# Kernel optimization log

Hardware: AMD Instinct MI355X
Metric: run time of the kernel (lower is better)

Reference implementation:

```python
import jax, jax.numpy as jnp
import numpy as np

N, IN, HID, OUT, HD = 512, 256, 256, 256, 64  # n_agents, in_dim, hid_dim, out_dim, head_dim (out_dim // n_heads)


def _mlp2(x, w1, b1, w2, b2):
    return jax.nn.relu(x @ w1.T + b1) @ w2.T + b2


def setup_inputs():
    key = jax.random.key(0)
    ks = jax.random.split(key, 32)
    p = lambda i, shape: jax.random.normal(ks[i], shape, dtype=jnp.float32) * 0.05
    V = jax.random.normal(ks[0], (N, IN), dtype=jnp.float32)
    adj = jax.random.randint(ks[1], (N, N), 0, 2, dtype=jnp.int32)
    adj = adj.at[jnp.arange(N), jnp.arange(N)].set(1)  # self-loops so no softmax row is all -inf
    prev_hidden = jax.random.normal(ks[2], (N, HID), dtype=jnp.float32)
    return {
        "V": V, "adj": adj, "prev_hidden": prev_hidden,
        "W1": p(3, (HID, IN)), "sa0": p(4, (HID,)), "sa1": p(5, (HID,)),
        "ce_w1": p(6, (HID, 2 * IN)), "ce_b1": p(7, (HID,)), "ce_w2": p(8, (HD, HID)), "ce_b2": p(9, (HD,)),
        "ca0": p(10, (HD,)), "ca1": p(11, (HD,)),
        "te_w1": p(12, (HID, IN + HID)), "te_b1": p(13, (HID,)), "te_w2": p(14, (HD, HID)), "te_b2": p(15, (HD,)),
        "ta0": p(16, (HD,)), "ta1": p(17, (HD,)),
        "pe_w1": p(18, (HID, 3 * IN)), "pe_b1": p(19, (HID,)), "pe_w2": p(20, (HD, HID)), "pe_b2": p(21, (HD,)),
        "pa0": p(22, (HD,)), "pa1": p(23, (HD,)),
        "W2": p(24, (OUT, HID + 2 * HD + 1)), "op_w": p(25, (OUT, OUT)), "op_b": p(26, (OUT,)),
        "ln_g": jnp.ones((OUT,), jnp.float32), "ln_b": jnp.zeros((OUT,), jnp.float32),
    }


def _forward(V, adj, prev_hidden, W1, sa0, sa1, ce_w1, ce_b1, ce_w2, ce_b2, ca0, ca1,
             te_w1, te_b1, te_w2, te_b2, ta0, ta1, pe_w1, pe_b1, pe_w2, pe_b2, pa0, pa1,
             W2, op_w, op_b, ln_g, ln_b):
    neg = -jnp.inf
    # --- branch 1: standard GAT attention ---
    Wh1 = V @ W1.T                                             # (N, HID)
    s1 = (Wh1 @ sa0)[:, None] + (Wh1 @ sa1)[None, :]           # (N, N)
    s1 = jnp.where(adj == 0, neg, s1)
    H1 = jax.nn.softmax(s1, axis=1) @ Wh1                      # (N, HID)
    # --- branch 2: causal, all ordered pairs i != j ---
    wA, wB = ce_w1[:, :IN], ce_w1[:, IN:]
    h = jax.nn.relu((V @ wA.T)[:, None, :] + (V @ wB.T)[None, :, :] + ce_b1)  # (N, N, HID)
    f = h @ ce_w2.T + ce_b2                                    # (N, N, HD)
    s2 = jnp.where(jnp.eye(N, dtype=bool), neg, f @ (ca0 + ca1))
    a2 = jax.nn.softmax(s2.reshape(-1)).reshape(N, N)          # softmax over all off-diagonal pairs
    H2 = jnp.broadcast_to(jnp.einsum('ij,ijd->d', a2, f), (N, HD))
    # --- branch 3: temporal; (N,1) scores broadcast against (N,N) causal mask ---
    tf = _mlp2(jnp.concatenate([V, prev_hidden], -1), te_w1, te_b1, te_w2, te_b2)  # (N, HD)
    ts = tf @ (ta0 + ta1)                                      # (N,)
    cmask = jnp.triu(jnp.ones((N, N), dtype=bool), 1)
    s3 = jnp.where(cmask, neg, jnp.broadcast_to(ts[:, None], (N, N)))
    H3 = jax.nn.softmax(s3, axis=1) @ tf                       # (N, HD) == prefix means of tf
    # --- branch 4: cooperative; first two neighbors in index order (zeros if < 2) ---
    pos = jnp.where(adj == 1, jnp.arange(N)[None, :], N)
    srt = jnp.sort(pos, axis=1)
    i0, i1 = srt[:, 0], srt[:, 1]
    valid = (i1 < N)[:, None]
    n0 = jnp.where(valid, V[jnp.clip(i0, 0, N - 1)], 0.0)
    n1 = jnp.where(valid, V[jnp.clip(i1, 0, N - 1)], 0.0)
    cf = _mlp2(jnp.concatenate([V, n0, n1], -1), pe_w1, pe_b1, pe_w2, pe_b2)  # (N, HD)
    # torch: softmax over dim of size 1 -> all ones, alpha^T @ cf == column sums -> (HD,)
    # then unsqueezed to (HD,1) and zero-padded to (N,1) since HD < N  (faithful to source bug)
    H4v = cf.sum(axis=0)
    H4 = jnp.concatenate([H4v, jnp.zeros((N - HD,), V.dtype)])[:, None]       # (N, 1)
    # --- combine ---
    Hc = jnp.concatenate([H1, H2, H3, H4], axis=-1) @ W2.T     # (N, OUT)
    out = Hc @ op_w.T + op_b
    mu = out.mean(-1, keepdims=True)
    var = ((out - mu) ** 2).mean(-1, keepdims=True)
    y = (out - mu) / jnp.sqrt(var + 1e-5) * ln_g + ln_b        # LayerNorm, eps=1e-5
    return jax.nn.elu(y)                                       # dropout is identity in eval


def reference(V, adj, prev_hidden, W1, sa0, sa1, ce_w1, ce_b1, ce_w2, ce_b2, ca0, ca1,
              te_w1, te_b1, te_w2, te_b2, ta0, ta1, pe_w1, pe_b1, pe_w2, pe_b2, pa0, pa1,
              W2, op_w, op_b, ln_g, ln_b):
    return _forward(V, adj, prev_hidden, W1, sa0, sa1, ce_w1, ce_b1, ce_w2, ce_b2, ca0, ca1,
                    te_w1, te_b1, te_w2, te_b2, ta0, ta1, pe_w1, pe_b1, pe_w2, pe_b2, pa0, pa1,
                    W2, op_w, op_b, ln_g, ln_b)
```

## Files before the change

### kernel.cpp

```cpp
#include <hip/hip_runtime.h>

typedef unsigned short u16;

constexpr int kN   = 512;
constexpr int kIN  = 256;
constexpr int kHID = 256;
constexpr int kHD  = 64;
constexpr int kOUT = 256;

__device__ __forceinline__ float us2f(u16 u){
  union { unsigned int i; float f; } c; c.i = ((unsigned int)u) << 16; return c.f;
}
__device__ __forceinline__ u16 f2us(float f){
  union { float f; unsigned int i; } c; c.f = f;
  unsigned int r = c.i + 0x7fff + ((c.i >> 16) & 1);
  return (u16)(r >> 16);
}

__device__ bool probe_is_f32(const unsigned int* __restrict__ V){
  __shared__ int cnt;
  if (threadIdx.x == 0) cnt = 0;
  __syncthreads();
  int c = 0;
  for (int k = threadIdx.x; k < 4096; k += 256){
    float x = us2f((u16)(V[k] & 0xffffu));
    if (!(fabsf(x) <= 32.0f)) c++;
  }
  atomicAdd(&cnt, c);
  __syncthreads();
  return cnt > 64;
}

struct ConvArgs { const void* src[23]; float* dst[23]; int n[23]; };

__global__ __launch_bounds__(256) void k_conv(ConvArgs a, const unsigned int* __restrict__ Vraw,
                                              const int* __restrict__ adj, int* __restrict__ flag,
                                              float* __restrict__ Xp)
{
  int b = blockIdx.x, tid = threadIdx.x;
  bool f32 = probe_is_f32(Vraw);
  if (b < 256){
    if (b == 0 && tid == 0) *flag = f32 ? 1 : 0;
    int t = b*256 + tid;
    const int stride = 65536;
    for (int s = 0; s < 23; ++s){
      int n4 = a.n[s] >> 2;
      float4* d = (float4*)a.dst[s];
      if (f32){
        const float4* sf = (const float4*)a.src[s];
        for (int i = t; i < n4; i += stride) d[i] = sf[i];
      } else {
        const ushort4* sb = (const ushort4*)a.src[s];
        for (int i = t; i < n4; i += stride){
          ushort4 u = sb[i];
          d[i] = make_float4(us2f(u.x), us2f(u.y), us2f(u.z), us2f(u.w));
        }
      }
    }
  } else {
    __shared__ unsigned long long msk[8];
    __shared__ int sj[2];
    int i = b - 256;
    int w = tid >> 6, lane = tid & 63;
    unsigned long long m0 = __ballot(adj[(size_t)i*kN + tid] != 0);
    unsigned long long m1 = __ballot(adj[(size_t)i*kN + 256 + tid] != 0);
    if (lane == 0){ msk[w] = m0; msk[4 + w] = m1; }
    __syncthreads();
    if (tid == 0){
      int j0 = -1, j1 = -1;
      for (int c = 0; c < 8 && j1 < 0; ++c){
        unsigned long long m = msk[c];
        while (m && j1 < 0){
          int bb = __builtin_ctzll(m);
          int j = c*64 + bb;
          if (j0 < 0) j0 = j; else j1 = j;
          m &= m - 1;
        }
      }
      if (j1 < 0) j0 = -1;
      sj[0] = j0; sj[1] = j1;
    }
    __syncthreads();
    int j0 = sj[0], j1 = sj[1];
    const float* Vf = (const float*)Vraw;
    const u16*  Vb = (const u16*)Vraw;
    auto rdV = [&](int r, int k)->float{
      return f32 ? Vf[(size_t)r*kIN + k] : us2f(Vb[(size_t)r*kIN + k]);
    };
    Xp[(size_t)i*768 + tid]       = rdV(i, tid);
    Xp[(size_t)i*768 + 256 + tid] = (j0 >= 0) ? rdV(j0, tid) : 0.f;
    Xp[(size_t)i*768 + 512 + tid] = (j1 >= 0) ? rdV(j1, tid) : 0.f;
  }
}

__device__ __forceinline__ float blk_red(float v, float* tmp, bool isMax){
  int lane = threadIdx.x & 63, wv = threadIdx.x >> 6;
  #pragma unroll
  for (int o = 32; o > 0; o >>= 1){
    float t = __shfl_down(v, o, 64);
    v = isMax ? fmaxf(v, t) : (v + t);
  }
  __syncthreads();
  if (lane == 0) tmp[wv] = v;
  __syncthreads();
  float r = tmp[0];
  for (int i = 1; i < 4; ++i) r = isMax ? fmaxf(r, tmp[i]) : (r + tmp[i]);
  return r;
}

struct WSP {
  const int* adj; const int* flag; void* out;
  float *Vf,*prevf,*W1f,*sa1f,*cw1f,*cb1f,*cw2f,*cb2f,*ca0f,*ca1f;
  float *tw1f,*tb1f,*tw2f,*tb2f,*pw1f,*pb1f,*pw2f,*pb2f;
  float *W2f,*opwf,*opbf,*lngf,*lnbf;
  float *tw2t,*pw2t,*W2c,*W2midt,*w384v,*c2v;
  float *Wh1,*e1v,*minv,*invzv,*H1p,*Hc,*Am,*Bm,*uvec,*beta;
  float *s2,*maxp,*zp,*MZ,*gsum;
  float *htp0,*htp1,*hpp0,*hpp1,*hpp2,*hidden_t,*hidden_p;
  float *tfm,*cfm,*H4v,*Xp,*out2,*out3;
};

struct GSeg2 { const float* X; const float* W; float* C; int ldx, ldw, ldc, K; };
struct GArgs2 { GSeg2 s[8]; };

__global__ __launch_bounds__(256) void k_gemmA(GArgs2 ga)
{
  __shared__ __align__(16) float Xs[2][32][68];
  __shared__ __align__(16) float Ws[2][32][68];
  const GSeg2 sg = ga.s[blockIdx.y];
  const int tm = blockIdx.x & 7;
  const int tn = blockIdx.x >> 3;
  const int i0 = tm << 6;
  const int n0 = tn << 6;
  const int tid = threadIdx.x;

  const int xrow = tid >> 3;
  const int xk   = (tid & 7) << 2;
  const int rg = (tid >> 4) << 2;
  const int cg = (tid & 15) << 2;

  const float* Xb = sg.X + (size_t)i0 * sg.ldx;
  const float* Wb = sg.W + (size_t)n0 * sg.ldw;

  float4 xr0, xr1, wr0, wr1;
  auto loadT = [&](int kt){
    xr0 = *(const float4*)(Xb + (size_t)xrow * sg.ldx + kt + xk);
    xr1 = *(const float4*)(Xb + (size_t)(xrow+32) * sg.ldx + kt + xk);
    wr0 = *(const float4*)(Wb + (size_t)xrow * sg.ldw + kt + xk);
    wr1 = *(const float4*)(Wb + (size_t)(xrow+32) * sg.ldw + kt + xk);
  };
  auto writeT = [&](int bu){
    Xs[bu][xk+0][xrow] = xr0.x;  Xs[bu][xk+1][xrow] = xr0.y;
    Xs[bu][xk+2][xrow] = xr0.z;  Xs[bu][xk+3][xrow] = xr0.w;
    Xs[bu][xk+0][xrow+32] = xr1.x;  Xs[bu][xk+1][xrow+32] = xr1.y;
    Xs[bu][xk+2][xrow+32] = xr1.z;  Xs[bu][xk+3][xrow+32] = xr1.w;
    Ws[bu][xk+0][xrow]    = wr0.x; Ws[bu][xk+1][xrow]    = wr0.y;
    Ws[bu][xk+2][xrow]    = wr0.z; Ws[bu][xk+3][xrow]    = wr0.w;
    Ws[bu][xk+0][xrow+32] = wr1.x; Ws[bu][xk+1][xrow+32] = wr1.y;
    Ws[bu][xk+2][xrow+32] = wr1.z; Ws[bu][xk+3][xrow+32] = wr1.w;
  };

  loadT(0); writeT(0); __syncthreads();

  float acc[4][4] = {};
  const int nkt = sg.K >> 5;
  for (int t = 0; t < nkt; ++t){
    if (t + 1 < nkt) loadT((t + 1) << 5);
    const int bu = t & 1;
    #pragma unroll
    for (int kk = 0; kk < 32; ++kk){
      const float4 av = *(const float4*)&Xs[bu][kk][rg];
      const float4 bv = *(const float4*)&Ws[bu][kk][cg];
      acc[0][0]+=av.x*bv.x; acc[0][1]+=av.x*bv.y; acc[0][2]+=av.x*bv.z; acc[0][3]+=av.x*bv.w;
      acc[1][0]+=av.y*bv.x; acc[1][1]+=av.y*bv.y; acc[1][2]+=av.y*bv.z; acc[1][3]+=av.y*bv.w;
      acc[2][0]+=av.z*bv.x; acc[2][1]+=av.z*bv.y; acc[2][2]+=av.z*bv.z; acc[2][3]+=av.z*bv.w;
      acc[3][0]+=av.w*bv.x; acc[3][1]+=av.w*bv.y; acc[3][2]+=av.w*bv.z; acc[3][3]+=av.w*bv.w;
    }
    if (t + 1 < nkt) writeT((t + 1) & 1);
    __syncthreads();
  }

  #pragma unroll
  for (int ri = 0; ri < 4; ++ri)
    *(float4*)(sg.C + (size_t)(i0 + rg + ri) * sg.ldc + (n0 + cg)) =
      make_float4(acc[ri][0], acc[ri][1], acc[ri][2], acc[ri][3]);
}

struct GS32 { const float* X; const float* W; float* C; int ldx, ldw, ldc, K;
              const float* c2; const float* w384; const float* h4; };

__device__ __forceinline__ void gemm32_body(const GS32 sg, int tm, int tn, int tid,
                                            float* Xs, float* Ws)
{
  const int i0 = tm << 5, n0 = tn << 5;
  const int xrow = tid >> 3;
  const int xk = (tid & 7) << 2;
  const int rg = (tid >> 4) << 1;
  const int cg = (tid & 15) << 1;
  const float* Xb = sg.X + (size_t)i0 * sg.ldx;
  const float* Wb = sg.W + (size_t)n0 * sg.ldw;
  float h4r = 0.f;
  if (sg.h4){ int i = i0 + xrow; h4r = (i < 64) ? sg.h4[i] : 0.f; }
  float4 xr, wr;
  auto loadT = [&](int kt){
    xr = *(const float4*)(Xb + (size_t)xrow * sg.ldx + kt + xk);
    wr = *(const float4*)(Wb + (size_t)xrow * sg.ldw + kt + xk);
    if (sg.c2){
      float4 c = *(const float4*)(sg.c2 + kt + xk);
      float4 w3 = *(const float4*)(sg.w384 + kt + xk);
      xr.x += c.x + h4r*w3.x; xr.y += c.y + h4r*w3.y;
      xr.z += c.z + h4r*w3.z; xr.w += c.w + h4r*w3.w;
    }
  };
  auto writeT = [&](int bu){
    float* xs = Xs + bu*1152;
    xs[(xk+0)*36 + xrow] = xr.x; xs[(xk+1)*36 + xrow] = xr.y;
    xs[(xk+2)*36 + xrow] = xr.z; xs[(xk+3)*36 + xrow] = xr.w;
    float* wsp = Ws + bu*1152;
    wsp[(xk+0)*36 + xrow] = wr.x; wsp[(xk+1)*36 + xrow] = wr.y;
    wsp[(xk+2)*36 + xrow] = wr.z; wsp[(xk+3)*36 + xrow] = wr.w;
  };
  loadT(0); writeT(0); __syncthreads();
  float a00=0,a01=0,a10=0,a11=0;
  const int nkt = sg.K >> 5;
  for (int t = 0; t < nkt; ++t){
    if (t+1 < nkt) loadT((t+1) << 5);
    const float* xs = Xs + (t&1)*1152;
    const float* wsp = Ws + (t&1)*1152;
    #pragma unroll
    for (int kk = 0; kk < 32; ++kk){
      float2 av = *(const float2*)&xs[kk*36 + rg];
      float2 bv = *(const float2*)&wsp[kk*36 + cg];
      a00 += av.x*bv.x; a01 += av.x*bv.y;
      a10 += av.y*bv.x; a11 += av.y*bv.y;
    }
    if (t+1 < nkt) writeT((t+1)&1);
    __syncthreads();
  }
  float* cp = sg.C + (size_t)(i0+rg)*sg.ldc + n0 + cg;
  *(float2*)cp = make_float2(a00, a01);
  *(float2*)(cp + sg.ldc) = make_float2(a10, a11);
}

__global__ __launch_bounds__(256) void k_stage2(WSP w)
{
  __shared__ float st[64*65];
  int b = blockIdx.x, tid = threadIdx.x;
  if (b < 128){
    int f = b*256 + tid;
    int c4 = f & 63;
    {
      float4 a = ((const float4*)w.htp0)[f], bb = ((const float4*)w.htp1)[f];
      float4 bi = ((const float4*)w.tb1f)[c4];
      ((float4*)w.hidden_t)[f] = make_float4(
        fmaxf(a.x+bb.x+bi.x,0.f), fmaxf(a.y+bb.y+bi.y,0.f),
        fmaxf(a.z+bb.z+bi.z,0.f), fmaxf(a.w+bb.w+bi.w,0.f));
    }
    {
      float4 a = ((const float4*)w.hpp0)[f], bb = ((const float4*)w.hpp1)[f];
      float4 c = ((const float4*)w.hpp2)[f];
      float4 bi = ((const float4*)w.pb1f)[c4];
      ((float4*)w.hidden_p)[f] = make_float4(
        fmaxf(a.x+bb.x+c.x+bi.x,0.f), fmaxf(a.y+bb.y+c.y+bi.y,0.f),
        fmaxf(a.z+bb.z+c.z+bi.z,0.f), fmaxf(a.w+bb.w+c.w+bi.w,0.f));
    }
  } else if (b < 256){
    int r = (b-128)*4 + (tid >> 6), lane = tid & 63;
    float a = 0.f;
    for (int k = lane; k < kHID; k += 64) a += w.Wh1[(size_t)r*kHID + k] * w.sa1f[k];
    #pragma unroll
    for (int o = 32; o > 0; o >>= 1) a += __shfl_down(a, o, 64);
    if (lane == 0) w.e1v[r] = a;
  } else if (b == 256){
    if (tid < 64){ st[tid] = w.ca0f[tid] + w.ca1f[tid]; w.H4v[tid] = 0.f; }
    __syncthreads();
    float a = 0.f;
    for (int d = 0; d < kHD; ++d) a += w.cw2f[(size_t)d*kHID + tid] * st[d];
    w.uvec[tid] = a;
    if (tid == 0){
      float bsum = 0.f;
      for (int d = 0; d < kHD; ++d) bsum += w.cb2f[d] * st[d];
      *w.beta = bsum;
    }
  } else if (b < 259){
    const float* src = (b == 257) ? w.tw2f : w.pw2f;
    float* dst = (b == 257) ? w.tw2t : w.pw2t;
    for (int ch = 0; ch < 4; ++ch){
      __syncthreads();
      #pragma unroll
      for (int e = 0; e < 16; ++e){
        int lin = e*256 + tid;
        int r = lin >> 6, c = lin & 63;
        st[r*65 + c] = src[(size_t)r*256 + ch*64 + c];
      }
      __syncthreads();
      #pragma unroll
      for (int e = 0; e < 16; ++e){
        int lin = e*256 + tid;
        int kc = lin >> 6, dd = lin & 63;
        dst[(size_t)(ch*64 + kc)*64 + dd] = st[dd*65 + kc];
      }
    }
  } else if (b < 323){
    int o0 = (b - 259) * 4;
    for (int r = 0; r < 4; ++r){
      int o = o0 + r;
      const float* src = w.W2f + (size_t)o * 385;
      float* dst = w.W2c + (size_t)o * 320;
      for (int c = tid; c < 320; c += 256)
        dst[c] = src[(c < 256) ? c : c + 64];
    }
  } else if (b < 339){
    int d0 = (b - 323) * 4;
    #pragma unroll
    for (int dd = 0; dd < 4; ++dd)
      w.W2midt[(size_t)(d0+dd)*256 + tid] = w.W2f[(size_t)tid*385 + 256 + d0 + dd];
  } else {
    w.w384v[tid] = w.W2f[(size_t)tid*385 + 384];
  }
}

__global__ __launch_bounds__(256) void k_stage3(WSP w)
{
  __shared__ __align__(16) float smem3[4*256 + 256];
  int b = blockIdx.x, tid = threadIdx.x;
  if (b < 64){
    int m = b >> 5, grp = b & 31;
    const float* X  = m ? w.hidden_p : w.hidden_t;
    const float* Wt = m ? w.pw2t : w.tw2t;
    const float* bi = m ? w.pb2f : w.tb2f;
    float* C = m ? w.cfm : w.tfm;
    int i0 = grp*16 + (tid >> 6)*4;
    int d = tid & 63;
    const float* x0 = X + (size_t)i0*256;
    const float* x1 = x0 + 256;
    const float* x2 = x0 + 512;
    const float* x3 = x0 + 768;
    float a0=0.f, a1=0.f, a2=0.f, a3=0.f;
    for (int k = 0; k < 256; k += 4){
      float w0 = Wt[(size_t)(k+0)*64 + d];
      float w1 = Wt[(size_t)(k+1)*64 + d];
      float w2 = Wt[(size_t)(k+2)*64 + d];
      float w3 = Wt[(size_t)(k+3)*64 + d];
      float4 f0 = *(const float4*)(x0 + k);
      float4 f1 = *(const float4*)(x1 + k);
      float4 f2 = *(const float4*)(x2 + k);
      float4 f3 = *(const float4*)(x3 + k);
      a0 += f0.x*w0 + f0.y*w1 + f0.z*w2 + f0.w*w3;
      a1 += f1.x*w0 + f1.y*w1 + f1.z*w2 + f1.w*w3;
      a2 += f2.x*w0 + f2.y*w1 + f2.z*w2 + f2.w*w3;
      a3 += f3.x*w0 + f3.y*w1 + f3.z*w2 + f3.w*w3;
    }
    float bd = bi[d];
    C[(size_t)(i0+0)*64 + d] = a0 + bd;
    C[(size_t)(i0+1)*64 + d] = a1 + bd;
    C[(size_t)(i0+2)*64 + d] = a2 + bd;
    C[(size_t)(i0+3)*64 + d] = a3 + bd;
  } else if (b < 576){
    float* red = smem3;
    int i = b - 64;
    int m0 = w.adj[(size_t)i*kN + tid];
    int m1 = w.adj[(size_t)i*kN + tid + 256];
    float ea = w.e1v[tid], eb = w.e1v[tid+256];
    float v0 = m0 ? ea : -1e30f;
    float v1 = m1 ? eb : -1e30f;
    float m = blk_red(fmaxf(v0, v1), red, true);
    float z = blk_red((m0 ? expf(ea-m) : 0.f) + (m1 ? expf(eb-m) : 0.f), red, false);
    if (tid == 0){ w.minv[i] = m; w.invzv[i] = 1.0f / z; }
  } else {
    float* aib = smem3;
    float* uu  = smem3 + 1024;
    int q = b - 576;
    int i0 = (q & 127) * 4, j0 = (q >> 7) * 64;
    int wv = tid >> 6, lane = tid & 63;
    uu[tid] = w.uvec[tid];
    float b1v = w.cb1f[tid];
    #pragma unroll
    for (int r = 0; r < 4; ++r) aib[r*256 + tid] = w.Am[(size_t)(i0+r)*kHID + tid] + b1v;
    __syncthreads();
    int i = i0 + wv, j = j0 + lane;
    const float4* bp = (const float4*)(w.Bm + (size_t)j*kHID);
    float acc = *w.beta;
    #pragma unroll 8
    for (int k4 = 0; k4 < kHID/4; ++k4){
      float4 bv = bp[k4];
      float4 a4 = *(const float4*)&aib[wv*256 + k4*4];
      float4 u4 = *(const float4*)&uu[k4*4];
      acc += fmaxf(a4.x+bv.x,0.f)*u4.x + fmaxf(a4.y+bv.y,0.f)*u4.y
           + fmaxf(a4.z+bv.z,0.f)*u4.z + fmaxf(a4.w+bv.w,0.f)*u4.w;
    }
    if (j == i) acc = -1e30f;
    w.s2[(size_t)i*kN + j] = acc;
    float m = acc;
    #pragma unroll
    for (int o = 32; o > 0; o >>= 1) m = fmaxf(m, __shfl_down(m, o, 64));
    m = __shfl(m, 0, 64);
    float e = expf(acc - m);
    #pragma unroll
    for (int o = 32; o > 0; o >>= 1) e += __shfl_down(e, o, 64);
    if (lane == 0){
      int pb = q*4 + wv;
      w.maxp[pb] = m; w.zp[pb] = e;
    }
  }
}

__global__ __launch_bounds__(256) void k_stage4(WSP w)
{
  __shared__ __align__(16) float smem[272];
  int b = blockIdx.x, tid = threadIdx.x;
  if (b < 8){
    int d = tid & 63, sub = tid >> 6;
    int r0 = b*64 + sub*16;
    float s = 0.f;
    #pragma unroll
    for (int e = 0; e < 16; ++e) s += w.cfm[(size_t)(r0+e)*kHD + d];
    smem[sub*64 + d] = s;
    __syncthreads();
    if (tid < 64)
      atomicAdd(&w.H4v[tid], smem[tid] + smem[64+tid] + smem[128+tid] + smem[192+tid]);
  } else if (b < 1032){
    float* wt = smem;
    int q = b - 8;
    int i0 = (q & 127) * 4, jt = q >> 7, j0 = jt * 64;
    {
      int r = tid >> 6, jj = tid & 63;
      int j = j0 + jj;
      wt[r*64 + jj] = w.adj[(size_t)(i0+r)*kN + j]
                    ? expf(w.e1v[j] - w.minv[i0+r]) * w.invzv[i0+r] : 0.f;
    }
    __syncthreads();
    float a0=0,a1=0,a2=0,a3=0;
    #pragma unroll 4
    for (int jj = 0; jj < 64; ++jj){
      float wh = w.Wh1[(size_t)(j0+jj)*kHID + tid];
      a0 += wt[jj]*wh; a1 += wt[64+jj]*wh; a2 += wt[128+jj]*wh; a3 += wt[192+jj]*wh;
    }
    size_t base = ((size_t)jt*kN + i0)*kHID + tid;
    w.H1p[base]          = a0;
    w.H1p[base + kHID]   = a1;
    w.H1p[base + 2*kHID] = a2;
    w.H1p[base + 3*kHID] = a3;
  } else {
    float* red = smem;
    float m = -1e30f;
    #pragma unroll
    for (int r = 0; r < 16; ++r) m = fmaxf(m, w.maxp[tid + 256*r]);
    m = blk_red(m, red, true);
    float z = 0.f;
    #pragma unroll
    for (int r = 0; r < 16; ++r) z += w.zp[tid + 256*r] * expf(w.maxp[tid + 256*r] - m);
    z = blk_red(z, red, false);
    if (tid == 0){ w.MZ[0] = m; w.MZ[1] = z; }
    w.gsum[tid] = 0.f;
  }
}

__global__ __launch_bounds__(256) void k_stage5(WSP w)
{
  __shared__ __align__(16) char smem[1536];
  int b = blockIdx.x, tid = threadIdx.x;
  if (b < 1024){
    float* wt = (float*)smem;
    int i0 = (b & 31) * 16, j0 = (b >> 5) * 16;
    float M = w.MZ[0], invZ = 1.0f / w.MZ[1];
    {
      int r = tid >> 4, c = tid & 15;
      wt[r*16 + c] = expf(w.s2[(size_t)(i0+r)*kN + (j0+c)] - M) * invZ;
    }
    float b1v = w.cb1f[tid];
    float aib[16];
    #pragma unroll
    for (int r = 0; r < 16; ++r) aib[r] = w.Am[(size_t)(i0+r)*kHID + tid] + b1v;
    __syncthreads();
    float acc = 0.f;
    for (int j = 0; j < 16; ++j){
      float bj = w.Bm[(size_t)(j0+j)*kHID + tid];
      #pragma unroll
      for (int r = 0; r < 16; ++r)
        acc += wt[r*16 + j] * fmaxf(aib[r] + bj, 0.f);
    }
    atomicAdd(&w.gsum[tid], acc);
  } else if (b < 1536){
    int i = b - 1024;
    float s = 0.f;
    #pragma unroll
    for (int jt = 0; jt < 8; ++jt)
      s += w.H1p[((size_t)jt*kN + i)*kHID + tid];
    w.Hc[(size_t)i*320 + tid] = s;
  } else {
    int d = b - 1536;
    int lane = tid & 63, wv = tid >> 6;
    float v0 = w.tfm[(size_t)(2*tid)*kHD + d];
    float v1 = w.tfm[(size_t)(2*tid+1)*kHD + d];
    float s = v0 + v1;
    float x = s;
    #pragma unroll
    for (int off = 1; off < 64; off <<= 1){
      float y = __shfl_up(x, off, 64);
      if (lane >= off) x += y;
    }
    float* wsum = (float*)smem;
    if (lane == 63) wsum[wv] = x;
    __syncthreads();
    float base = 0.f;
    for (int k = 0; k < wv; ++k) base += wsum[k];
    float excl = base + x - s;
    w.Hc[(size_t)(2*tid)*320 + 256 + d]   = (excl + v0) / (float)(2*tid + 1);
    w.Hc[(size_t)(2*tid+1)*320 + 256 + d] = (excl + s)  / (float)(2*tid + 2);
  }
}

__global__ __launch_bounds__(256) void k_out2g(WSP w)
{
  __shared__ __align__(16) char smem[18432];
  int b = blockIdx.x, tid = threadIdx.x;
  if (b < 128){
    GS32 sg{w.Hc, w.W2c, w.out2, 320, 320, 256, 320, nullptr, nullptr, nullptr};
    gemm32_body(sg, b & 15, b >> 4, tid, (float*)smem, (float*)(smem + 9216));
  } else {
    float* gs  = (float*)smem;
    float* part= (float*)(smem + 1024);
    float* h2s = (float*)(smem + 2048);
    gs[tid] = w.gsum[tid];
    __syncthreads();
    int dd = tid >> 2, q = tid & 3;
    float a = 0.f;
    for (int kk = 0; kk < 64; ++kk){
      int k = q*64 + kk;
      a += gs[k] * w.cw2f[(size_t)dd*kHID + k];
    }
    part[dd*4 + q] = a;
    __syncthreads();
    if (tid < kHD)
      h2s[tid] = w.cb2f[tid] + part[tid*4] + part[tid*4+1] + part[tid*4+2] + part[tid*4+3];
    __syncthreads();
    float c = 0.f;
    for (int d = 0; d < kHD; ++d) c += h2s[d] * w.W2midt[(size_t)d*256 + tid];
    w.c2v[tid] = c;
  }
}

__global__ __launch_bounds__(256) void k_out3g(WSP w)
{
  __shared__ __align__(16) char smem[18432];
  GS32 sg{w.out2, w.opwf, w.out3, 256, 256, 256, 256, w.c2v, w.w384v, w.H4v};
  gemm32_body(sg, blockIdx.x & 15, blockIdx.x >> 4, threadIdx.x, (float*)smem, (float*)(smem + 9216));
}

__global__ __launch_bounds__(256) void k_final(WSP w)
{
  int b = blockIdx.x, tid = threadIdx.x;
  int row = b*4 + (tid >> 6), lane = tid & 63;
  float4 v = *(const float4*)(w.out3 + (size_t)row*kOUT + lane*4);
  float4 pb = *(const float4*)(w.opbf + lane*4);
  v.x += pb.x; v.y += pb.y; v.z += pb.z; v.w += pb.w;
  float s = v.x + v.y + v.z + v.w;
  #pragma unroll
  for (int o = 32; o > 0; o >>= 1) s += __shfl_xor(s, o, 64);
  float mu = s * (1.0f/kOUT);
  float dx = v.x-mu, dy = v.y-mu, dz = v.z-mu, dw = v.w-mu;
  float ss = dx*dx + dy*dy + dz*dz + dw*dw;
  #pragma unroll
  for (int o = 32; o > 0; o >>= 1) ss += __shfl_xor(ss, o, 64);
  float rs = rsqrtf(ss * (1.0f/kOUT) + 1e-5f);
  float4 g = *(const float4*)(w.lngf + lane*4);
  float4 be = *(const float4*)(w.lnbf + lane*4);
  float y0 = dx*rs*g.x + be.x, y1 = dy*rs*g.y + be.y;
  float y2 = dz*rs*g.z + be.z, y3 = dw*rs*g.w + be.w;
  y0 = (y0 > 0.f) ? y0 : expm1f(y0);
  y1 = (y1 > 0.f) ? y1 : expm1f(y1);
  y2 = (y2 > 0.f) ? y2 : expm1f(y2);
  y3 = (y3 > 0.f) ? y3 : expm1f(y3);
  if (*w.flag){
    *(float4*)((float*)w.out + (size_t)row*kOUT + lane*4) = make_float4(y0,y1,y2,y3);
  } else {
    ushort4 u; u.x = f2us(y0); u.y = f2us(y1); u.z = f2us(y2); u.w = f2us(y3);
    ((ushort4*)w.out)[(size_t)row*64 + lane] = u;
  }
}

extern "C" void kernel_launch(void* const* d_in, const int* in_sizes, int n_in,
                              void* d_out, int out_size, void* d_ws, size_t ws_size,
                              hipStream_t stream)
{
  const void* V     = d_in[0];
  const int*  adj   = (const int*)d_in[1];
  const void* prev  = d_in[2];
  const void* W1    = d_in[3];
  const void* sa1   = d_in[5];
  const void* ce_w1 = d_in[6];
  const void* ce_b1 = d_in[7];
  const void* ce_w2 = d_in[8];
  const void* ce_b2 = d_in[9];
  const void* ca0   = d_in[10];
  const void* ca1   = d_in[11];
  const void* te_w1 = d_in[12];
  const void* te_b1 = d_in[13];
  const void* te_w2 = d_in[14];
  const void* te_b2 = d_in[15];
  const void* pe_w1 = d_in[18];
  const void* pe_b1 = d_in[19];
  const void* pe_w2 = d_in[20];
  const void* pe_b2 = d_in[21];
  const void* W2    = d_in[24];
  const void* op_w  = d_in[25];
  const void* op_b  = d_in[26];
  const void* ln_g  = d_in[27];
  const void* ln_b  = d_in[28];

  float* ws  = (float*)d_ws;
  int*  flag = (int*)ws;
  float* p   = ws + 16;
  float* Vf   = p; p += 131072;
  float* prevf= p; p += 131072;
  float* W1f  = p; p += 65536;
  float* sa1f = p; p += 256;
  float* cw1f = p; p += 131072;
  float* cb1f = p; p += 256;
  float* cw2f = p; p += 16384;
  float* cb2f = p; p += 64;
  float* ca0f = p; p += 64;
  float* ca1f = p; p += 64;
  float* tw1f = p; p += 131072;
  float* tb1f = p; p += 256;
  float* tw2f = p; p += 16384;
  float* tb2f = p; p += 64;
  float* pw1f = p; p += 196608;
  float* pb1f = p; p += 256;
  float* pw2f = p; p += 16384;
  float* pb2f = p; p += 64;
  float* W2f  = p; p += 98560;
  float* opwf = p; p += 65536;
  float* opbf = p; p += 256;
  float* lngf = p; p += 256;
  float* lnbf = p; p += 256;
  float* tw2t = p; p += 16384;
  float* pw2t = p; p += 16384;
  float* W2c  = p; p += 81920;
  float* W2midt = p; p += 16384;
  float* w384v  = p; p += 256;
  float* c2v    = p; p += 256;
  float* Wh1      = p; p += 131072;
  float* e1v      = p; p += 512;
  float* minv     = p; p += 512;
  float* invzv    = p; p += 512;
  float* H1p      = p; p += 1048576;
  float* Hc       = p; p += 163840;
  float* Am       = p; p += 131072;
  float* Bm       = p; p += 131072;
  float* uvec     = p; p += 256;
  float* beta     = p; p += 16;
  float* s2       = p; p += 262144;
  float* maxp     = p; p += 4096;
  float* zpart    = p; p += 4096;
  float* MZ       = p; p += 16;
  float* gsum     = p; p += 256;
  float* htp0     = p; p += 131072;
  float* htp1     = p; p += 131072;
  float* hpp0     = p; p += 131072;
  float* hpp1     = p; p += 131072;
  float* hpp2     = p; p += 131072;
  float* hidden_t = p; p += 131072;
  float* hidden_p = p; p += 131072;
  float* tfm      = p; p += 32768;
  float* cfm      = p; p += 32768;
  float* H4v      = p; p += 64;
  float* Xp       = p; p += 393216;
  float* out2     = p; p += 131072;
  float* out3     = p; p += 131072;

  WSP w;
  w.adj = adj; w.flag = flag; w.out = d_out;
  w.Vf=Vf; w.prevf=prevf; w.W1f=W1f; w.sa1f=sa1f; w.cw1f=cw1f; w.cb1f=cb1f;
  w.cw2f=cw2f; w.cb2f=cb2f; w.ca0f=ca0f; w.ca1f=ca1f;
  w.tw1f=tw1f; w.tb1f=tb1f; w.tw2f=tw2f; w.tb2f=tb2f;
  w.pw1f=pw1f; w.pb1f=pb1f; w.pw2f=pw2f; w.pb2f=pb2f;
  w.W2f=W2f; w.opwf=opwf; w.opbf=opbf; w.lngf=lngf; w.lnbf=lnbf;
  w.tw2t=tw2t; w.pw2t=pw2t; w.W2c=W2c; w.W2midt=W2midt; w.w384v=w384v; w.c2v=c2v;
  w.Wh1=Wh1; w.e1v=e1v; w.minv=minv; w.invzv=invzv; w.H1p=H1p; w.Hc=Hc;
  w.Am=Am; w.Bm=Bm; w.uvec=uvec; w.beta=beta;
  w.s2=s2; w.maxp=maxp; w.zp=zpart; w.MZ=MZ; w.gsum=gsum;
  w.htp0=htp0; w.htp1=htp1; w.hpp0=hpp0; w.hpp1=hpp1; w.hpp2=hpp2;
  w.hidden_t=hidden_t; w.hidden_p=hidden_p;
  w.tfm=tfm; w.cfm=cfm; w.H4v=H4v; w.Xp=Xp; w.out2=out2; w.out3=out3;

  {
    ConvArgs ca;
    const void* srcs[23] = {V, prev, W1, sa1, ce_w1, ce_b1, ce_w2, ce_b2, ca0, ca1,
                            te_w1, te_b1, te_w2, te_b2, pe_w1, pe_b1, pe_w2, pe_b2,
                            W2, op_w, op_b, ln_g, ln_b};
    float* dsts[23] = {Vf, prevf, W1f, sa1f, cw1f, cb1f, cw2f, cb2f, ca0f, ca1f,
                       tw1f, tb1f, tw2f, tb2f, pw1f, pb1f, pw2f, pb2f,
                       W2f, opwf, opbf, lngf, lnbf};
    int ns[23] = {131072, 131072, 65536, 256, 131072, 256, 16384, 64, 64, 64,
                  131072, 256, 16384, 64, 196608, 256, 16384, 64,
                  98560, 65536, 256, 256, 256};
    for (int s = 0; s < 23; ++s){ ca.src[s] = srcs[s]; ca.dst[s] = dsts[s]; ca.n[s] = ns[s]; }
    k_conv<<<768, 256, 0, stream>>>(ca, (const unsigned int*)V, adj, flag, Xp);
  }

  {
    GArgs2 g{};
    g.s[0] = {Vf,       W1f,        Wh1,  256, 256, 256, 256};
    g.s[1] = {Vf,       cw1f,       Am,   256, 512, 256, 256};
    g.s[2] = {Vf,       cw1f + 256, Bm,   256, 512, 256, 256};
    g.s[3] = {Vf,       tw1f,       htp0, 256, 512, 256, 256};
    g.s[4] = {prevf,    tw1f + 256, htp1, 256, 512, 256, 256};
    g.s[5] = {Xp,       pw1f,       hpp0, 768, 768, 256, 256};
    g.s[6] = {Xp + 256, pw1f + 256, hpp1, 768, 768, 256, 256};
    g.s[7] = {Xp + 512, pw1f + 512, hpp2, 768, 768, 256, 256};
    k_gemmA<<<dim3(32, 8), 256, 0, stream>>>(g);
  }

  k_stage2<<<340, 256, 0, stream>>>(w);

  k_stage3<<<1600, 256, 0, stream>>>(w);

  k_stage4<<<1033, 256, 0, stream>>>(w);

  k_stage5<<<1600, 256, 0, stream>>>(w);

  k_out2g<<<129, 256, 0, stream>>>(w);

  k_out3g<<<128, 256, 0, stream>>>(w);

  k_final<<<128, 256, 0, stream>>>(w);
}
```

Measured before the change: 244.7 us.

## Compute GAT branch as softmax-weight matrix times Wh1 GEMM, fuse e1 into gemmA

The e1 = Wh1·sa1 dot products are now accumulated with atomics in the epilogue of the Wh1 GEMM, and the per-row softmax max and sum move into stage2. Stage3 writes a dense normalized attention matrix. H1 is then computed by a tiled GEMM (with a new K-major weight load path) straight into Hc, replacing the 8-way partial products and the separate reduction pass. This removes the large H1p scratch buffer and its reduction. In exchange it adds a 512x512 weight matrix write, float atomics that make e1 summation order nondeterministic, and a launch reordering that puts the out2 GEMM in stage5 with a separate single-block k_h2c.

```diff
diff --git a/kernel.cpp b/kernel.cpp
--- a/kernel.cpp
+++ b/kernel.cpp
@@ -35,12 +35,15 @@
 
 __global__ __launch_bounds__(256) void k_conv(ConvArgs a, const unsigned int* __restrict__ Vraw,
                                               const int* __restrict__ adj, int* __restrict__ flag,
-                                              float* __restrict__ Xp)
+                                              float* __restrict__ Xp, float* __restrict__ e1v)
 {
   int b = blockIdx.x, tid = threadIdx.x;
   bool f32 = probe_is_f32(Vraw);
   if (b < 256){
-    if (b == 0 && tid == 0) *flag = f32 ? 1 : 0;
+    if (b == 0){
+      if (tid == 0) *flag = f32 ? 1 : 0;
+      e1v[tid] = 0.f; e1v[tid + 256] = 0.f;
+    }
     int t = b*256 + tid;
     const int stride = 65536;
     for (int s = 0; s < 23; ++s){
@@ -114,14 +117,14 @@
   float *tw1f,*tb1f,*tw2f,*tb2f,*pw1f,*pb1f,*pw2f,*pb2f;
   float *W2f,*opwf,*opbf,*lngf,*lnbf;
   float *tw2t,*pw2t,*W2c,*W2midt,*w384v,*c2v;
-  float *Wh1,*e1v,*minv,*invzv,*H1p,*Hc,*Am,*Bm,*uvec,*beta;
+  float *Wh1,*e1v,*minv,*invzv,*wadj,*Hc,*Am,*Bm,*uvec,*beta;
   float *s2,*maxp,*zp,*MZ,*gsum;
   float *htp0,*htp1,*hpp0,*hpp1,*hpp2,*hidden_t,*hidden_p;
   float *tfm,*cfm,*H4v,*Xp,*out2,*out3;
 };
 
 struct GSeg2 { const float* X; const float* W; float* C; int ldx, ldw, ldc, K; };
-struct GArgs2 { GSeg2 s[8]; };
+struct GArgs2 { GSeg2 s[8]; const float* sa1; float* e1; };
 
 __global__ __launch_bounds__(256) void k_gemmA(GArgs2 ga)
 {
@@ -184,10 +187,24 @@
   for (int ri = 0; ri < 4; ++ri)
     *(float4*)(sg.C + (size_t)(i0 + rg + ri) * sg.ldc + (n0 + cg)) =
       make_float4(acc[ri][0], acc[ri][1], acc[ri][2], acc[ri][3]);
+
+  if (blockIdx.y == 0){
+    int cb = n0 + cg;
+    float s0 = ga.sa1[cb], s1 = ga.sa1[cb+1], s2v = ga.sa1[cb+2], s3 = ga.sa1[cb+3];
+    #pragma unroll
+    for (int ri = 0; ri < 4; ++ri){
+      float v = acc[ri][0]*s0 + acc[ri][1]*s1 + acc[ri][2]*s2v + acc[ri][3]*s3;
+      v += __shfl_xor(v, 1, 16);
+      v += __shfl_xor(v, 2, 16);
+      v += __shfl_xor(v, 4, 16);
+      v += __shfl_xor(v, 8, 16);
+      if ((tid & 15) == 0) atomicAdd(&ga.e1[i0 + rg + ri], v);
+    }
+  }
 }
 
 struct GS32 { const float* X; const float* W; float* C; int ldx, ldw, ldc, K;
-              const float* c2; const float* w384; const float* h4; };
+              const float* c2; const float* w384; const float* h4; int bkn; };
 
 __device__ __forceinline__ void gemm32_body(const GS32 sg, int tm, int tn, int tid,
                                             float* Xs, float* Ws)
@@ -198,13 +215,14 @@
   const int rg = (tid >> 4) << 1;
   const int cg = (tid & 15) << 1;
   const float* Xb = sg.X + (size_t)i0 * sg.ldx;
-  const float* Wb = sg.W + (size_t)n0 * sg.ldw;
+  const float* Wb = sg.bkn ? (sg.W + n0) : (sg.W + (size_t)n0 * sg.ldw);
   float h4r = 0.f;
   if (sg.h4){ int i = i0 + xrow; h4r = (i < 64) ? sg.h4[i] : 0.f; }
   float4 xr, wr;
   auto loadT = [&](int kt){
     xr = *(const float4*)(Xb + (size_t)xrow * sg.ldx + kt + xk);
-    wr = *(const float4*)(Wb + (size_t)xrow * sg.ldw + kt + xk);
+    if (sg.bkn) wr = *(const float4*)(Wb + (size_t)(kt + xrow) * sg.ldw + xk);
+    else        wr = *(const float4*)(Wb + (size_t)xrow * sg.ldw + kt + xk);
     if (sg.c2){
       float4 c = *(const float4*)(sg.c2 + kt + xk);
       float4 w3 = *(const float4*)(sg.w384 + kt + xk);
@@ -217,8 +235,13 @@
     xs[(xk+0)*36 + xrow] = xr.x; xs[(xk+1)*36 + xrow] = xr.y;
     xs[(xk+2)*36 + xrow] = xr.z; xs[(xk+3)*36 + xrow] = xr.w;
     float* wsp = Ws + bu*1152;
-    wsp[(xk+0)*36 + xrow] = wr.x; wsp[(xk+1)*36 + xrow] = wr.y;
-    wsp[(xk+2)*36 + xrow] = wr.z; wsp[(xk+3)*36 + xrow] = wr.w;
+    if (sg.bkn){
+      wsp[xrow*36 + xk+0] = wr.x; wsp[xrow*36 + xk+1] = wr.y;
+      wsp[xrow*36 + xk+2] = wr.z; wsp[xrow*36 + xk+3] = wr.w;
+    } else {
+      wsp[(xk+0)*36 + xrow] = wr.x; wsp[(xk+1)*36 + xrow] = wr.y;
+      wsp[(xk+2)*36 + xrow] = wr.z; wsp[(xk+3)*36 + xrow] = wr.w;
+    }
   };
   loadT(0); writeT(0); __syncthreads();
   float a00=0,a01=0,a10=0,a11=0;
@@ -264,14 +287,18 @@
         fmaxf(a.x+bb.x+c.x+bi.x,0.f), fmaxf(a.y+bb.y+c.y+bi.y,0.f),
         fmaxf(a.z+bb.z+c.z+bi.z,0.f), fmaxf(a.w+bb.w+c.w+bi.w,0.f));
     }
-  } else if (b < 256){
-    int r = (b-128)*4 + (tid >> 6), lane = tid & 63;
-    float a = 0.f;
-    for (int k = lane; k < kHID; k += 64) a += w.Wh1[(size_t)r*kHID + k] * w.sa1f[k];
-    #pragma unroll
-    for (int o = 32; o > 0; o >>= 1) a += __shfl_down(a, o, 64);
-    if (lane == 0) w.e1v[r] = a;
-  } else if (b == 256){
+  } else if (b < 640){
+    float* red = st;
+    int i = b - 128;
+    int m0 = w.adj[(size_t)i*kN + tid];
+    int m1 = w.adj[(size_t)i*kN + tid + 256];
+    float ea = w.e1v[tid], eb = w.e1v[tid+256];
+    float v0 = m0 ? ea : -1e30f;
+    float v1 = m1 ? eb : -1e30f;
+    float m = blk_red(fmaxf(v0, v1), red, true);
+    float z = blk_red((m0 ? expf(ea-m) : 0.f) + (m1 ? expf(eb-m) : 0.f), red, false);
+    if (tid == 0){ w.minv[i] = m; w.invzv[i] = 1.0f / z; }
+  } else if (b == 640){
     if (tid < 64){ st[tid] = w.ca0f[tid] + w.ca1f[tid]; w.H4v[tid] = 0.f; }
     __syncthreads();
     float a = 0.f;
@@ -282,9 +309,9 @@
       for (int d = 0; d < kHD; ++d) bsum += w.cb2f[d] * st[d];
       *w.beta = bsum;
     }
-  } else if (b < 259){
-    const float* src = (b == 257) ? w.tw2f : w.pw2f;
-    float* dst = (b == 257) ? w.tw2t : w.pw2t;
+  } else if (b < 643){
+    const float* src = (b == 641) ? w.tw2f : w.pw2f;
+    float* dst = (b == 641) ? w.tw2t : w.pw2t;
     for (int ch = 0; ch < 4; ++ch){
       __syncthreads();
       #pragma unroll
@@ -301,8 +328,8 @@
         dst[(size_t)(ch*64 + kc)*64 + dd] = st[dd*65 + kc];
       }
     }
-  } else if (b < 323){
-    int o0 = (b - 259) * 4;
+  } else if (b < 707){
+    int o0 = (b - 643) * 4;
     for (int r = 0; r < 4; ++r){
       int o = o0 + r;
       const float* src = w.W2f + (size_t)o * 385;
@@ -310,8 +337,8 @@
       for (int c = tid; c < 320; c += 256)
         dst[c] = src[(c < 256) ? c : c + 64];
     }
-  } else if (b < 339){
-    int d0 = (b - 323) * 4;
+  } else if (b < 723){
+    int d0 = (b - 707) * 4;
     #pragma unroll
     for (int dd = 0; dd < 4; ++dd)
       w.W2midt[(size_t)(d0+dd)*256 + tid] = w.W2f[(size_t)tid*385 + 256 + d0 + dd];
@@ -357,16 +384,12 @@
     C[(size_t)(i0+2)*64 + d] = a2 + bd;
     C[(size_t)(i0+3)*64 + d] = a3 + bd;
   } else if (b < 576){
-    float* red = smem3;
     int i = b - 64;
-    int m0 = w.adj[(size_t)i*kN + tid];
-    int m1 = w.adj[(size_t)i*kN + tid + 256];
-    float ea = w.e1v[tid], eb = w.e1v[tid+256];
-    float v0 = m0 ? ea : -1e30f;
-    float v1 = m1 ? eb : -1e30f;
-    float m = blk_red(fmaxf(v0, v1), red, true);
-    float z = blk_red((m0 ? expf(ea-m) : 0.f) + (m1 ? expf(eb-m) : 0.f), red, false);
-    if (tid == 0){ w.minv[i] = m; w.invzv[i] = 1.0f / z; }
+    float mi = w.minv[i], zi = w.invzv[i];
+    w.wadj[(size_t)i*kN + tid] =
+      w.adj[(size_t)i*kN + tid] ? expf(w.e1v[tid] - mi) * zi : 0.f;
+    w.wadj[(size_t)i*kN + tid + 256] =
+      w.adj[(size_t)i*kN + tid + 256] ? expf(w.e1v[tid+256] - mi) * zi : 0.f;
   } else {
     float* aib = smem3;
     float* uu  = smem3 + 1024;
@@ -407,42 +430,44 @@
 
 __global__ __launch_bounds__(256) void k_stage4(WSP w)
 {
-  __shared__ __align__(16) float smem[272];
+  __shared__ __align__(16) char smem[18432];
   int b = blockIdx.x, tid = threadIdx.x;
-  if (b < 8){
+  if (b < 128){
+    GS32 sg{w.wadj, w.Wh1, w.Hc, 512, 256, 320, 512, nullptr, nullptr, nullptr, 1};
+    gemm32_body(sg, b & 15, b >> 4, tid, (float*)smem, (float*)(smem + 9216));
+  } else if (b < 192){
+    int d = b - 128;
+    int lane = tid & 63, wv = tid >> 6;
+    float v0 = w.tfm[(size_t)(2*tid)*kHD + d];
+    float v1 = w.tfm[(size_t)(2*tid+1)*kHD + d];
+    float s = v0 + v1;
+    float x = s;
+    #pragma unroll
+    for (int off = 1; off < 64; off <<= 1){
+      float y = __shfl_up(x, off, 64);
+      if (lane >= off) x += y;
+    }
+    float* wsum = (float*)smem;
+    if (lane == 63) wsum[wv] = x;
+    __syncthreads();
+    float base = 0.f;
+    for (int k = 0; k < wv; ++k) base += wsum[k];
+    float excl = base + x - s;
+    w.Hc[(size_t)(2*tid)*320 + 256 + d]   = (excl + v0) / (float)(2*tid + 1);
+    w.Hc[(size_t)(2*tid+1)*320 + 256 + d] = (excl + s)  / (float)(2*tid + 2);
+  } else if (b < 200){
+    float* sm = (float*)smem;
     int d = tid & 63, sub = tid >> 6;
-    int r0 = b*64 + sub*16;
+    int r0 = (b-192)*64 + sub*16;
     float s = 0.f;
     #pragma unroll
     for (int e = 0; e < 16; ++e) s += w.cfm[(size_t)(r0+e)*kHD + d];
-    smem[sub*64 + d] = s;
+    sm[sub*64 + d] = s;
     __syncthreads();
     if (tid < 64)
-      atomicAdd(&w.H4v[tid], smem[tid] + smem[64+tid] + smem[128+tid] + smem[192+tid]);
-  } else if (b < 1032){
-    float* wt = smem;
-    int q = b - 8;
-    int i0 = (q & 127) * 4, jt = q >> 7, j0 = jt * 64;
-    {
-      int r = tid >> 6, jj = tid & 63;
-      int j = j0 + jj;
-      wt[r*64 + jj] = w.adj[(size_t)(i0+r)*kN + j]
-                    ? expf(w.e1v[j] - w.minv[i0+r]) * w.invzv[i0+r] : 0.f;
-    }
-    __syncthreads();
-    float a0=0,a1=0,a2=0,a3=0;
-    #pragma unroll 4
-    for (int jj = 0; jj < 64; ++jj){
-      float wh = w.Wh1[(size_t)(j0+jj)*kHID + tid];
-      a0 += wt[jj]*wh; a1 += wt[64+jj]*wh; a2 += wt[128+jj]*wh; a3 += wt[192+jj]*wh;
-    }
-    size_t base = ((size_t)jt*kN + i0)*kHID + tid;
-    w.H1p[base]          = a0;
-    w.H1p[base + kHID]   = a1;
-    w.H1p[base + 2*kHID] = a2;
-    w.H1p[base + 3*kHID] = a3;
+      atomicAdd(&w.H4v[tid], sm[tid] + sm[64+tid] + sm[128+tid] + sm[192+tid]);
   } else {
-    float* red = smem;
+    float* red = (float*)smem;
     float m = -1e30f;
     #pragma unroll
     for (int r = 0; r < 16; ++r) m = fmaxf(m, w.maxp[tid + 256*r]);
@@ -458,7 +483,7 @@
 
 __global__ __launch_bounds__(256) void k_stage5(WSP w)
 {
-  __shared__ __align__(16) char smem[1536];
+  __shared__ __align__(16) char smem[18432];
   int b = blockIdx.x, tid = threadIdx.x;
   if (b < 1024){
     float* wt = (float*)smem;
@@ -481,70 +506,41 @@
         acc += wt[r*16 + j] * fmaxf(aib[r] + bj, 0.f);
     }
     atomicAdd(&w.gsum[tid], acc);
-  } else if (b < 1536){
-    int i = b - 1024;
-    float s = 0.f;
-    #pragma unroll
-    for (int jt = 0; jt < 8; ++jt)
-      s += w.H1p[((size_t)jt*kN + i)*kHID + tid];
-    w.Hc[(size_t)i*320 + tid] = s;
   } else {
-    int d = b - 1536;
-    int lane = tid & 63, wv = tid >> 6;
-    float v0 = w.tfm[(size_t)(2*tid)*kHD + d];
-    float v1 = w.tfm[(size_t)(2*tid+1)*kHD + d];
-    float s = v0 + v1;
-    float x = s;
-    #pragma unroll
-    for (int off = 1; off < 64; off <<= 1){
-      float y = __shfl_up(x, off, 64);
-      if (lane >= off) x += y;
-    }
-    float* wsum = (float*)smem;
-    if (lane == 63) wsum[wv] = x;
-    __syncthreads();
-    float base = 0.f;
-    for (int k = 0; k < wv; ++k) base += wsum[k];
-    float excl = base + x - s;
-    w.Hc[(size_t)(2*tid)*320 + 256 + d]   = (excl + v0) / (float)(2*tid + 1);
-    w.Hc[(size_t)(2*tid+1)*320 + 256 + d] = (excl + s)  / (float)(2*tid + 2);
-  }
-}
-
-__global__ __launch_bounds__(256) void k_out2g(WSP w)
+    int q = b - 1024;
+    GS32 sg{w.Hc, w.W2c, w.out2, 320, 320, 256, 320, nullptr, nullptr, nullptr, 0};
+    gemm32_body(sg, q & 15, q >> 4, tid, (float*)smem, (float*)(smem + 9216));
+  }
+}
+
+__global__ void k_h2c(WSP w)
+{
+  __shared__ float gs[kHID];
+  __shared__ float part[kHD][4];
+  __shared__ float h2s[kHD];
+  int tid = threadIdx.x;
+  gs[tid] = w.gsum[tid];
+  __syncthreads();
+  int dd = tid >> 2, q = tid & 3;
+  float a = 0.f;
+  for (int kk = 0; kk < 64; ++kk){
+    int k = q*64 + kk;
+    a += gs[k] * w.cw2f[(size_t)dd*kHID + k];
+  }
+  part[dd][q] = a;
+  __syncthreads();
+  if (tid < kHD)
+    h2s[tid] = w.cb2f[tid] + part[tid][0] + part[tid][1] + part[tid][2] + part[tid][3];
+  __syncthreads();
+  float c = 0.f;
+  for (int d = 0; d < kHD; ++d) c += h2s[d] * w.W2midt[(size_t)d*256 + tid];
+  w.c2v[tid] = c;
+}
+
+__global__ __launch_bounds__(256) void k_out3g(WSP w)
 {
   __shared__ __align__(16) char smem[18432];
-  int b = blockIdx.x, tid = threadIdx.x;
-  if (b < 128){
-    GS32 sg{w.Hc, w.W2c, w.out2, 320, 320, 256, 320, nullptr, nullptr, nullptr};
-    gemm32_body(sg, b & 15, b >> 4, tid, (float*)smem, (float*)(smem + 9216));
-  } else {
-    float* gs  = (float*)smem;
-    float* part= (float*)(smem + 1024);
-    float* h2s = (float*)(smem + 2048);
-    gs[tid] = w.gsum[tid];
-    __syncthreads();
-    int dd = tid >> 2, q = tid & 3;
-    float a = 0.f;
-    for (int kk = 0; kk < 64; ++kk){
-      int k = q*64 + kk;
-      a += gs[k] * w.cw2f[(size_t)dd*kHID + k];
-    }
-    part[dd*4 + q] = a;
-    __syncthreads();
-    if (tid < kHD)
-      h2s[tid] = w.cb2f[tid] + part[tid*4] + part[tid*4+1] + part[tid*4+2] + part[tid*4+3];
-    __syncthreads();
-    float c = 0.f;
-    for (int d = 0; d < kHD; ++d) c += h2s[d] * w.W2midt[(size_t)d*256 + tid];
-    w.c2v[tid] = c;
-  }
-}
-
-__global__ __launch_bounds__(256) void k_out3g(WSP w)
-{
-  __shared__ __align__(16) char smem[18432];
-  GS32 sg{w.out2, w.opwf, w.out3, 256, 256, 256, 256, w.c2v, w.w384v, w.H4v};
+  GS32 sg{w.out2, w.opwf, w.out3, 256, 256, 256, 256, w.c2v, w.w384v, w.H4v, 0};
   gemm32_body(sg, blockIdx.x & 15, blockIdx.x >> 4, threadIdx.x, (float*)smem, (float*)(smem + 9216));
 }
 
@@ -645,7 +641,7 @@
   float* e1v      = p; p += 512;
   float* minv     = p; p += 512;
   float* invzv    = p; p += 512;
-  float* H1p      = p; p += 1048576;
+  float* wadj     = p; p += 262144;
   float* Hc       = p; p += 163840;
   float* Am       = p; p += 131072;
   float* Bm       = p; p += 131072;
@@ -678,7 +674,7 @@
   w.pw1f=pw1f; w.pb1f=pb1f; w.pw2f=pw2f; w.pb2f=pb2f;
   w.W2f=W2f; w.opwf=opwf; w.opbf=opbf; w.lngf=lngf; w.lnbf=lnbf;
   w.tw2t=tw2t; w.pw2t=pw2t; w.W2c=W2c; w.W2midt=W2midt; w.w384v=w384v; w.c2v=c2v;
-  w.Wh1=Wh1; w.e1v=e1v; w.minv=minv; w.invzv=invzv; w.H1p=H1p; w.Hc=Hc;
+  w.Wh1=Wh1; w.e1v=e1v; w.minv=minv; w.invzv=invzv; w.wadj=wadj; w.Hc=Hc;
   w.Am=Am; w.Bm=Bm; w.uvec=uvec; w.beta=beta;
   w.s2=s2; w.maxp=maxp; w.zp=zpart; w.MZ=MZ; w.gsum=gsum;
   w.htp0=htp0; w.htp1=htp1; w.hpp0=hpp0; w.hpp1=hpp1; w.hpp2=hpp2;
@@ -697,7 +693,7 @@
                   131072, 256, 16384, 64, 196608, 256, 16384, 64,
                   98560, 65536, 256, 256, 256};
     for (int s = 0; s < 23; ++s){ ca.src[s] = srcs[s]; ca.dst[s] = dsts[s]; ca.n[s] = ns[s]; }
-    k_conv<<<768, 256, 0, stream>>>(ca, (const unsigned int*)V, adj, flag, Xp);
+    k_conv<<<768, 256, 0, stream>>>(ca, (const unsigned int*)V, adj, flag, Xp, e1v);
   }
 
   {
@@ -710,18 +706,19 @@
     g.s[5] = {Xp,       pw1f,       hpp0, 768, 768, 256, 256};
     g.s[6] = {Xp + 256, pw1f + 256, hpp1, 768, 768, 256, 256};
     g.s[7] = {Xp + 512, pw1f + 512, hpp2, 768, 768, 256, 256};
+    g.sa1 = sa1f; g.e1 = e1v;
     k_gemmA<<<dim3(32, 8), 256, 0, stream>>>(g);
   }
 
-  k_stage2<<<340, 256, 0, stream>>>(w);
+  k_stage2<<<724, 256, 0, stream>>>(w);
 
   k_stage3<<<1600, 256, 0, stream>>>(w);
 
-  k_stage4<<<1033, 256, 0, stream>>>(w);
-
-  k_stage5<<<1600, 256, 0, stream>>>(w);
-
-  k_out2g<<<129, 256, 0, stream>>>(w);
+  k_stage4<<<201, 256, 0, stream>>>(w);
+
+  k_stage5<<<1152, 256, 0, stream>>>(w);
+
+  k_h2c<<<1, 256, 0, stream>>>(w);
 
   k_out3g<<<128, 256, 0, stream>>>(w);
 
```

Measured after the change: 243.5 us. Within noise of the previous version (-0.5%).
